# Performance work log

Measured on AMD Instinct MI355X. Metric: run time of the kernel, lower is better.

## Reference

```python
import jax, jax.numpy as jnp
import numpy as np


def _resize_bilinear_ac(x, oh, ow):
    """Bilinear resize with align_corners=True for NCHW input."""
    ih, iw = x.shape[-2], x.shape[-1]
    ys = jnp.linspace(0.0, ih - 1.0, oh)
    xs = jnp.linspace(0.0, iw - 1.0, ow)
    y0 = jnp.floor(ys).astype(jnp.int32)
    y1 = jnp.minimum(y0 + 1, ih - 1)
    wy = (ys - y0).astype(x.dtype)[None, None, :, None]
    x0 = jnp.floor(xs).astype(jnp.int32)
    x1 = jnp.minimum(x0 + 1, iw - 1)
    wx = (xs - x0).astype(x.dtype)[None, None, None, :]
    top = x[:, :, y0, :] * (1 - wy) + x[:, :, y1, :] * wy  # (B,1,oh,iw)
    return top[:, :, :, x0] * (1 - wx) + top[:, :, :, x1] * wx  # (B,1,oh,ow)


def raw_to_rgb_bg(image):
    """Demosaic a (*,1,H,W) bayer raw image, CFA.BG layout (top-left red)."""
    orig_shape = image.shape
    H, W = image.shape[-2], image.shape[-1]
    img = image.reshape(-1, 1, H, W)

    # CFA.BG: red at even rows/cols, blue at odd rows/cols
    r = img[:, :, ::2, ::2]   # (B,1,H/2,W/2)
    b = img[:, :, 1::2, 1::2]
    # rpad=(0,1,0,1): pad right/bottom by 1; bpad=(1,0,1,0): pad left/top by 1 (replicate)
    rpadded = jnp.pad(r, ((0, 0), (0, 0), (0, 1), (0, 1)), mode='edge')
    bpadded = jnp.pad(b, ((0, 0), (0, 0), (1, 0), (1, 0)), mode='edge')

    ru = _resize_bilinear_ac(rpadded, H + 1, W + 1)
    bu = _resize_bilinear_ac(bpadded, H + 1, W + 1)
    # negative padding = crop back to (H, W)
    ru = ru[:, :, :H, :W]      # crop right/bottom
    bu = bu[:, :, 1:, 1:]      # crop left/top

    # green: reflect-pad and apply fixed cross kernel (4-neighbour average)
    gp = jnp.pad(img, ((0, 0), (0, 0), (1, 1), (1, 1)), mode='reflect')
    gu = 0.25 * (gp[:, :, :-2, 1:-1] + gp[:, :, 2:, 1:-1]
                 + gp[:, :, 1:-1, :-2] + gp[:, :, 1:-1, 2:])
    # overwrite known green samples (CFA.BG: green at (even,odd) and (odd,even))
    gu = gu.at[:, :, ::2, 1::2].set(img[:, :, ::2, 1::2])
    gu = gu.at[:, :, 1::2, ::2].set(img[:, :, 1::2, ::2])

    ru = ru.reshape(orig_shape)
    gu = gu.reshape(orig_shape)
    bu = bu.reshape(orig_shape)
    return jnp.concatenate([ru, gu, bu], axis=-3)


def setup_inputs() -> dict:
    key = jax.random.key(0)
    image = jax.random.uniform(key, (8, 1, 2048, 2048), dtype=jnp.float32)
    return {"image": image}


def reference(image):
    return raw_to_rgb_bg(image)
```

## Files before the change

### kernel.cpp

```cpp
#include <hip/hip_runtime.h>


#define HH 2048
#define WW 2048

__global__ __launch_bounds__(256) void demosaic_bg_kernel(const float* __restrict__ in,
                                                          float* __restrict__ out) {
    const int strips_per_row = WW / 4;

    int bid = (int)blockIdx.x;
    int nb = (bid & 7) * ((int)gridDim.x >> 3) + (bid >> 3);
    int gid = nb * 256 + (int)threadIdx.x;

    int s = gid & (strips_per_row - 1);
    int t = gid >> 9;
    int yp = t & (HH / 2 - 1);
    int bimg = t >> 10;
    int y = yp << 1;
    int x0 = s << 2;
    int lane = (int)threadIdx.x & 63;

    const float* __restrict__ img = in + (size_t)bimg * HH * WW;

    const int i0 = (y == 0) ? 1 : y - 1;
    const int i3 = (y + 2 > HH - 2) ? (HH - 2) : y + 2;

    const float* pa = img + (size_t)i0 * WW;
    const float* pb = img + (size_t)y * WW;
    const float* pc = img + (size_t)(y + 1) * WW;
    const float* pd = img + (size_t)i3 * WW;

    float4 a = *(const float4*)(pa + x0);
    float4 b = *(const float4*)(pb + x0);
    float4 c = *(const float4*)(pc + x0);
    float4 d = *(const float4*)(pd + x0);

    float la = __shfl_up(a.w, 1);
    float lb = __shfl_up(b.w, 1);
    float lc = __shfl_up(c.w, 1);
    float rb = __shfl_down(b.x, 1);
    float rc = __shfl_down(c.x, 1);
    float rd = __shfl_down(d.x, 1);

    if (lane == 0) {
        if (x0 == 0) {
            la = a.y; lb = b.y; lc = c.y;
        } else {
            la = pa[x0 - 1]; lb = pb[x0 - 1]; lc = pc[x0 - 1];
        }
    }
    if (lane == 63) {
        if (x0 + 4 > WW - 2) {
            rb = b.z; rc = c.z; rd = d.z;
        } else {
            rb = pb[x0 + 4]; rc = pc[x0 + 4]; rd = pd[x0 + 4];
        }
    }

    float4 Re, Ge, Be;
    Re.x = b.x;
    Ge.x = 0.25f * (a.x + c.x + lb + b.y);
    Be.x = 0.25f * (la + a.y + lc + c.y);

    Re.y = 0.5f * (b.x + b.z);
    Ge.y = b.y;
    Be.y = 0.5f * (a.y + c.y);

    Re.z = b.z;
    Ge.z = 0.25f * (a.z + c.z + b.y + b.w);
    Be.z = 0.25f * (a.y + a.w + c.y + c.w);

    Re.w = 0.5f * (b.z + rb);
    Ge.w = b.w;
    Be.w = 0.5f * (a.w + c.w);

    float4 Ro, Go, Bo;
    Ro.x = 0.5f * (b.x + d.x);
    Go.x = c.x;
    Bo.x = 0.5f * (lc + c.y);

    Ro.y = 0.25f * (b.x + b.z + d.x + d.z);
    Go.y = 0.25f * (b.y + d.y + c.x + c.z);
    Bo.y = c.y;

    Ro.z = 0.5f * (b.z + d.z);
    Go.z = c.z;
    Bo.z = 0.5f * (c.y + c.w);

    Ro.w = 0.25f * (b.z + rb + d.z + rd);
    Go.w = 0.25f * (b.w + d.w + c.z + rc);
    Bo.w = c.w;

    const size_t plane = (size_t)HH * WW;
    size_t obase = (size_t)bimg * 3 * plane + (size_t)y * WW + x0;
    *(float4*)(out + obase)                  = Re;
    *(float4*)(out + obase + WW)             = Ro;
    *(float4*)(out + obase + plane)          = Ge;
    *(float4*)(out + obase + plane + WW)     = Go;
    *(float4*)(out + obase + 2 * plane)      = Be;
    *(float4*)(out + obase + 2 * plane + WW) = Bo;
}

extern "C" void kernel_launch(void* const* d_in, const int* in_sizes, int n_in,
                              void* d_out, int out_size, void* d_ws, size_t ws_size,
                              hipStream_t stream) {
    const float* in = (const float*)d_in[0];
    float* out = (float*)d_out;
    const int threads = 8 * (HH / 2) * (WW / 4);
    dim3 block(256);
    dim3 grid(threads / 256);
    demosaic_bg_kernel<<<grid, block, 0, stream>>>(in, out);
}
```

Before: 485.8 us.

## Loop each thread over all batch images with software-prefetched loads

Each thread now handles the same spatial strip across all eight images in an unrolled loop, and prefetches the next image's four rows while computing the current one. The grid shrinks eightfold, which amortises index math and boundary setup and adds memory-level parallelism per thread. The cost is higher register use and fewer resident waves, which could reduce latency hiding in what is a bandwidth-bound kernel. The block-swizzle mapping now spans only spatial positions.

```diff
diff --git a/kernel.cpp b/kernel.cpp
--- a/kernel.cpp
+++ b/kernel.cpp
@@ -3,102 +3,113 @@
 
 #define HH 2048
 #define WW 2048
+#define NIMG 8
 
 __global__ __launch_bounds__(256) void demosaic_bg_kernel(const float* __restrict__ in,
                                                           float* __restrict__ out) {
-    const int strips_per_row = WW / 4;
+    const size_t IMG   = (size_t)HH * WW;
+    const size_t PLANE = (size_t)HH * WW;
+    const size_t OIMG  = 3 * PLANE;
 
     int bid = (int)blockIdx.x;
     int nb = (bid & 7) * ((int)gridDim.x >> 3) + (bid >> 3);
     int gid = nb * 256 + (int)threadIdx.x;
 
-    int s = gid & (strips_per_row - 1);
-    int t = gid >> 9;
-    int yp = t & (HH / 2 - 1);
-    int bimg = t >> 10;
-    int y = yp << 1;
+    int s  = gid & 511;
+    int yp = gid >> 9;
+    int y  = yp << 1;
     int x0 = s << 2;
     int lane = (int)threadIdx.x & 63;
-
-    const float* __restrict__ img = in + (size_t)bimg * HH * WW;
 
     const int i0 = (y == 0) ? 1 : y - 1;
     const int i3 = (y + 2 > HH - 2) ? (HH - 2) : y + 2;
 
-    const float* pa = img + (size_t)i0 * WW;
-    const float* pb = img + (size_t)y * WW;
-    const float* pc = img + (size_t)(y + 1) * WW;
-    const float* pd = img + (size_t)i3 * WW;
+    const float* pa = in + (size_t)i0 * WW + x0;
+    const float* pb = in + (size_t)y * WW + x0;
+    const float* pc = in + (size_t)(y + 1) * WW + x0;
+    const float* pd = in + (size_t)i3 * WW + x0;
+    float* op = out + (size_t)y * WW + x0;
 
-    float4 a = *(const float4*)(pa + x0);
-    float4 b = *(const float4*)(pb + x0);
-    float4 c = *(const float4*)(pc + x0);
-    float4 d = *(const float4*)(pd + x0);
+    const bool lz  = (lane == 0);
+    const bool l63 = (lane == 63);
+    const bool xlo = (x0 == 0);
+    const bool xhi = (x0 + 4 > WW - 2);
 
-    float la = __shfl_up(a.w, 1);
-    float lb = __shfl_up(b.w, 1);
-    float lc = __shfl_up(c.w, 1);
-    float rb = __shfl_down(b.x, 1);
-    float rc = __shfl_down(c.x, 1);
-    float rd = __shfl_down(d.x, 1);
+    float4 a = *(const float4*)pa;
+    float4 b = *(const float4*)pb;
+    float4 c = *(const float4*)pc;
+    float4 d = *(const float4*)pd;
 
-    if (lane == 0) {
-        if (x0 == 0) {
-            la = a.y; lb = b.y; lc = c.y;
-        } else {
-            la = pa[x0 - 1]; lb = pb[x0 - 1]; lc = pc[x0 - 1];
+#pragma unroll
+    for (int k = 0; k < NIMG; ++k) {
+        float4 fa, fb, fc, fd;
+        if (k + 1 < NIMG) {
+            fa = *(const float4*)(pa + IMG);
+            fb = *(const float4*)(pb + IMG);
+            fc = *(const float4*)(pc + IMG);
+            fd = *(const float4*)(pd + IMG);
         }
+
+        float la = __shfl_up(a.w, 1);
+        float lb = __shfl_up(b.w, 1);
+        float lc = __shfl_up(c.w, 1);
+        float rb = __shfl_down(b.x, 1);
+        float rc = __shfl_down(c.x, 1);
+        float rd = __shfl_down(d.x, 1);
+
+        if (lz) {
+            if (xlo) { la = a.y; lb = b.y; lc = c.y; }
+            else     { la = pa[-1]; lb = pb[-1]; lc = pc[-1]; }
+        }
+        if (l63) {
+            if (xhi) { rb = b.z; rc = c.z; rd = d.z; }
+            else     { rb = pb[4]; rc = pc[4]; rd = pd[4]; }
+        }
+
+        float4 Re, Ge, Be;
+        Re.x = b.x;
+        Ge.x = 0.25f * (a.x + c.x + lb + b.y);
+        Be.x = 0.25f * (la + a.y + lc + c.y);
+
+        Re.y = 0.5f * (b.x + b.z);
+        Ge.y = b.y;
+        Be.y = 0.5f * (a.y + c.y);
+
+        Re.z = b.z;
+        Ge.z = 0.25f * (a.z + c.z + b.y + b.w);
+        Be.z = 0.25f * (a.y + a.w + c.y + c.w);
+
+        Re.w = 0.5f * (b.z + rb);
+        Ge.w = b.w;
+        Be.w = 0.5f * (a.w + c.w);
+
+        float4 Ro, Go, Bo;
+        Ro.x = 0.5f * (b.x + d.x);
+        Go.x = c.x;
+        Bo.x = 0.5f * (lc + c.y);
+
+        Ro.y = 0.25f * (b.x + b.z + d.x + d.z);
+        Go.y = 0.25f * (b.y + d.y + c.x + c.z);
+        Bo.y = c.y;
+
+        Ro.z = 0.5f * (b.z + d.z);
+        Go.z = c.z;
+        Bo.z = 0.5f * (c.y + c.w);
+
+        Ro.w = 0.25f * (b.z + rb + d.z + rd);
+        Go.w = 0.25f * (b.w + d.w + c.z + rc);
+        Bo.w = c.w;
+
+        *(float4*)(op)                  = Re;
+        *(float4*)(op + WW)             = Ro;
+        *(float4*)(op + PLANE)          = Ge;
+        *(float4*)(op + PLANE + WW)     = Go;
+        *(float4*)(op + 2 * PLANE)      = Be;
+        *(float4*)(op + 2 * PLANE + WW) = Bo;
+
+        pa += IMG; pb += IMG; pc += IMG; pd += IMG; op += OIMG;
+        if (k + 1 < NIMG) { a = fa; b = fb; c = fc; d = fd; }
     }
-    if (lane == 63) {
-        if (x0 + 4 > WW - 2) {
-            rb = b.z; rc = c.z; rd = d.z;
-        } else {
-            rb = pb[x0 + 4]; rc = pc[x0 + 4]; rd = pd[x0 + 4];
-        }
-    }
-
-    float4 Re, Ge, Be;
-    Re.x = b.x;
-    Ge.x = 0.25f * (a.x + c.x + lb + b.y);
-    Be.x = 0.25f * (la + a.y + lc + c.y);
-
-    Re.y = 0.5f * (b.x + b.z);
-    Ge.y = b.y;
-    Be.y = 0.5f * (a.y + c.y);
-
-    Re.z = b.z;
-    Ge.z = 0.25f * (a.z + c.z + b.y + b.w);
-    Be.z = 0.25f * (a.y + a.w + c.y + c.w);
-
-    Re.w = 0.5f * (b.z + rb);
-    Ge.w = b.w;
-    Be.w = 0.5f * (a.w + c.w);
-
-    float4 Ro, Go, Bo;
-    Ro.x = 0.5f * (b.x + d.x);
-    Go.x = c.x;
-    Bo.x = 0.5f * (lc + c.y);
-
-    Ro.y = 0.25f * (b.x + b.z + d.x + d.z);
-    Go.y = 0.25f * (b.y + d.y + c.x + c.z);
-    Bo.y = c.y;
-
-    Ro.z = 0.5f * (b.z + d.z);
-    Go.z = c.z;
-    Bo.z = 0.5f * (c.y + c.w);
-
-    Ro.w = 0.25f * (b.z + rb + d.z + rd);
-    Go.w = 0.25f * (b.w + d.w + c.z + rc);
-    Bo.w = c.w;
-
-    const size_t plane = (size_t)HH * WW;
-    size_t obase = (size_t)bimg * 3 * plane + (size_t)y * WW + x0;
-    *(float4*)(out + obase)                  = Re;
-    *(float4*)(out + obase + WW)             = Ro;
-    *(float4*)(out + obase + plane)          = Ge;
-    *(float4*)(out + obase + plane + WW)     = Go;
-    *(float4*)(out + obase + 2 * plane)      = Be;
-    *(float4*)(out + obase + 2 * plane + WW) = Bo;
 }
 
 extern "C" void kernel_launch(void* const* d_in, const int* in_sizes, int n_in,
@@ -106,8 +117,7 @@
                               hipStream_t stream) {
     const float* in = (const float*)d_in[0];
     float* out = (float*)d_out;
-    const int threads = 8 * (HH / 2) * (WW / 4);
     dim3 block(256);
-    dim3 grid(threads / 256);
+    dim3 grid((HH / 2) * (WW / 4) / 256);
     demosaic_bg_kernel<<<grid, block, 0, stream>>>(in, out);
 }
```

Result: no change. 492.5 us (+1.4%).
